# Optimization experiments

Measured on AMD Instinct MI355X. Metric: run time of the kernel, lower is better.

## Reference

```python
import jax, jax.numpy as jnp
import numpy as np

EPS = 1e-8


def setup_inputs() -> dict:
    key = jax.random.key(0)
    k1, k2, k3, k4 = jax.random.split(key, 4)
    B, S, H, D, E = 2, 2048, 1024, 4096, 8
    x = jax.random.normal(k1, (B, S, H), dtype=jnp.float32)
    routing_weights = jax.random.uniform(k2, (B, S, E), dtype=jnp.float32)
    # xavier-uniform-like scale for the expert weight tensors
    lim_d = float(np.sqrt(6.0 / (H + D)))
    lim_u = float(np.sqrt(6.0 / (D + H)))
    down_weights = jax.random.uniform(k3, (E, H, D), dtype=jnp.float32, minval=-lim_d, maxval=lim_d)
    up_weights = jax.random.uniform(k4, (E, D, H), dtype=jnp.float32, minval=-lim_u, maxval=lim_u)
    down_biases = jnp.zeros((E, D), dtype=jnp.float32)
    return {
        "x": x,
        "routing_weights": routing_weights,
        "down_weights": down_weights,
        "down_biases": down_biases,
        "up_weights": up_weights,
        "top_k": 2,
    }


def reference(x, routing_weights, down_weights, down_biases, up_weights, top_k):
    """SmearExpert.forward with routing_strategy='top_k_sparse' (3D routing weights).
    Returns (output, sparse_weights) exactly as the torch module does."""
    B, S, H = x.shape
    E = down_weights.shape[0]

    # top-k sparsification + renormalization of the routing weights
    topk_w, topk_i = jax.lax.top_k(routing_weights, top_k)          # [B,S,k]
    sparse_w = (jax.nn.one_hot(topk_i, E, dtype=x.dtype) * topk_w[..., None]).sum(-2)  # [B,S,E]
    sparse_w = sparse_w / (sparse_w.sum(-1, keepdims=True) + EPS)

    x_flat = x.reshape(-1, H)              # [T,H]
    w_flat = sparse_w.reshape(-1, E)       # [T,E]

    # per-expert down-proj -> GELU(exact) -> up-proj, combined with routing weights
    # (tokens with zero weight contribute nothing, matching the masked torch path)
    out = jnp.zeros_like(x_flat)
    for e in range(E):
        z = jax.nn.gelu(x_flat @ down_weights[e] + down_biases[e], approximate=False)  # [T,D]
        out = out + (z @ up_weights[e]) * w_flat[:, e:e + 1]
    return out.reshape(B, S, H), sparse_w
```

## Files before the change

### kernel.cpp

```cpp
#include <hip/hip_runtime.h>
#include <stdint.h>

#define T_TOK 4096
#define HDIM  1024
#define DDIM  4096
#define NEXP  8

typedef unsigned short ushort_t;
typedef __attribute__((ext_vector_type(8))) short bf16x8;
typedef __attribute__((ext_vector_type(4))) float f32x4;

__device__ __forceinline__ float bf2f(ushort_t b) {
  return __uint_as_float(((unsigned int)b) << 16);
}
__device__ __forceinline__ unsigned int f2bf(float f) {
  unsigned int u = __float_as_uint(f);
  return (u + 0x7fffu + ((u >> 16) & 1u)) >> 16;
}

__device__ __forceinline__ void gld16(const void* g, void* l) {
  __builtin_amdgcn_global_load_lds(
      (const __attribute__((address_space(1))) unsigned int*)g,
      (__attribute__((address_space(3))) unsigned int*)l, 16, 0, 0);
}

__global__ void k_init(int* counts) {
  if (threadIdx.x < NEXP) counts[threadIdx.x] = 0;
}

__global__ void k_route(const float* __restrict__ rw, float* __restrict__ sw_out,
                        int* counts, int* inv_e, int* inv_p, float* inv_w,
                        int* tokA) {
  int t = blockIdx.x * 256 + threadIdx.x;
  if (t >= T_TOK) return;
  float v[NEXP];
#pragma unroll
  for (int e = 0; e < NEXP; e++) v[e] = rw[t * NEXP + e];
  int i0 = 0; float m0 = v[0];
#pragma unroll
  for (int e = 1; e < NEXP; e++) if (v[e] > m0) { m0 = v[e]; i0 = e; }
  int i1 = -1; float m1 = -1e30f;
#pragma unroll
  for (int e = 0; e < NEXP; e++) if (e != i0 && v[e] > m1) { m1 = v[e]; i1 = e; }
  float s = m0 + m1 + 1e-8f;
  float w0 = m0 / s, w1 = m1 / s;
#pragma unroll
  for (int e = 0; e < NEXP; e++) {
    float w = (e == i0) ? w0 : ((e == i1) ? w1 : 0.0f);
    sw_out[t * NEXP + e] = w;
  }
  int p0 = atomicAdd(&counts[i0], 1);
  int p1 = atomicAdd(&counts[i1], 1);
  tokA[i0 * T_TOK + p0] = t;
  tokA[i1 * T_TOK + p1] = t;
  inv_e[t * 2] = i0; inv_e[t * 2 + 1] = i1;
  inv_p[t * 2] = p0; inv_p[t * 2 + 1] = p1;
  inv_w[t * 2] = w0; inv_w[t * 2 + 1] = w1;
}

__global__ void k_offsets(const int* counts, int* offsets) {
  int acc = 0;
  for (int e = 0; e < NEXP; e++) { offsets[e] = acc; acc += counts[e]; }
}

__global__ __launch_bounds__(256)
void k_cvtx(const float* __restrict__ x, ushort_t* __restrict__ xb) {
  size_t i = (size_t)blockIdx.x * 256 + threadIdx.x;
  float4 f0 = ((const float4*)x)[i * 2];
  float4 f1 = ((const float4*)x)[i * 2 + 1];
  uint4 o;
  o.x = f2bf(f0.x) | (f2bf(f0.y) << 16);
  o.y = f2bf(f0.z) | (f2bf(f0.w) << 16);
  o.z = f2bf(f1.x) | (f2bf(f1.y) << 16);
  o.w = f2bf(f1.z) | (f2bf(f1.w) << 16);
  ((uint4*)xb)[i] = o;
}

template <int KDIM, int NDIM>
__global__ __launch_bounds__(256)
void k_cvtw(const float* __restrict__ W, ushort_t* __restrict__ Wt) {
  constexpr int KT = KDIM / 64;
  __shared__ __align__(16) ushort_t lds[64 * 256];
  const int ekt = blockIdx.y;
  const int e  = ekt / KT;
  const int kt = ekt % KT;
  const int n0 = blockIdx.x * 256;
  const int t  = threadIdx.x;
  const int wv = t >> 6;
  const int ln = t & 63;
  const float* src = W + (size_t)e * KDIM * NDIM + (size_t)(kt * 64) * NDIM + n0;
#pragma unroll
  for (int it = 0; it < 16; ++it) {
    int r = it * 4 + wv;
    float4 f = *(const float4*)(src + (size_t)r * NDIM + ln * 4);
    uint2 o;
    o.x = f2bf(f.x) | (f2bf(f.y) << 16);
    o.y = f2bf(f.z) | (f2bf(f.w) << 16);
    *(uint2*)(lds + r * 256 + ln * 4) = o;
  }
  __syncthreads();
  ushort_t* dst = Wt + ((size_t)ekt * NDIM + n0 + t) * 64;
  const int sw = t & 7;
#pragma unroll
  for (int g = 0; g < 8; ++g) {
    unsigned int h0 = lds[(g * 8 + 0) * 256 + t];
    unsigned int h1 = lds[(g * 8 + 1) * 256 + t];
    unsigned int h2 = lds[(g * 8 + 2) * 256 + t];
    unsigned int h3 = lds[(g * 8 + 3) * 256 + t];
    unsigned int h4 = lds[(g * 8 + 4) * 256 + t];
    unsigned int h5 = lds[(g * 8 + 5) * 256 + t];
    unsigned int h6 = lds[(g * 8 + 6) * 256 + t];
    unsigned int h7 = lds[(g * 8 + 7) * 256 + t];
    uint4 o;
    o.x = h0 | (h1 << 16);
    o.y = h2 | (h3 << 16);
    o.z = h4 | (h5 << 16);
    o.w = h6 | (h7 << 16);
    *(uint4*)(dst + (g ^ sw) * 8) = o;
  }
}

template <int KDIM, int NDIM, bool DOWN>
__global__ __launch_bounds__(256, 3)
void k_gemm(const ushort_t* __restrict__ Asrc, const ushort_t* __restrict__ Wt,
            const float* __restrict__ bias, const int* __restrict__ counts,
            const int* __restrict__ offsets, const int* __restrict__ tokA,
            ushort_t* __restrict__ Out) {
  constexpr int KT = KDIM / 64;
  __shared__ __align__(16) short a_sh[128 * 64];
  __shared__ __align__(16) short b_sh[128 * 64];
  const int e    = blockIdx.y >> 5;
  const int tile = blockIdx.y & 31;
  const int cnt  = counts[e];
  if (tile * 128 >= cnt) return;
  const int off_e = offsets[e];
  const int zbase = off_e + tile * 128;
  const int n0    = blockIdx.x * 128;
  const int tid   = threadIdx.x;
  const int wave  = tid >> 6;
  const int lane  = tid & 63;
  const int rgrp  = lane >> 3;
  const int lc    = lane & 7;

  const ushort_t* abase[4];
#pragma unroll
  for (int i = 0; i < 4; i++) {
    int rl = wave * 32 + i * 8 + rgrp;
    int ridx = tile * 128 + rl;
    int ridx_c = (ridx < cnt) ? ridx : tile * 128;
    size_t row;
    if constexpr (DOWN) row = (size_t)tokA[e * T_TOK + ridx_c];
    else                row = (size_t)(off_e + ridx_c);
    abase[i] = Asrc + row * KDIM + ((lc ^ (rl & 7)) * 8);
  }
  const ushort_t* bbase = Wt + ((size_t)e * KT * NDIM + n0) * 64 + wave * 2048 + lane * 8;
  char* a_seg = (char*)a_sh + wave * 4096;
  char* b_seg = (char*)b_sh + wave * 4096;

  const int lm   = lane & 15;
  const int quad = lane >> 4;

  f32x4 acc[8][2];
  const f32x4 zero = {0.0f, 0.0f, 0.0f, 0.0f};
#pragma unroll
  for (int mf = 0; mf < 8; mf++)
#pragma unroll
    for (int nf = 0; nf < 2; nf++) acc[mf][nf] = zero;

  for (int kt = 0; kt < KT; ++kt) {
#pragma unroll
    for (int it = 0; it < 4; ++it)
      gld16(abase[it] + kt * 64, a_seg + it * 1024);
    const ushort_t* bg = bbase + (size_t)kt * (NDIM * 64);
#pragma unroll
    for (int it = 0; it < 4; ++it)
      gld16(bg + it * 512, b_seg + it * 1024);
    __syncthreads();
#pragma unroll
    for (int ks = 0; ks < 2; ++ks) {
      bf16x8 af[8];
#pragma unroll
      for (int mf = 0; mf < 8; mf++) {
        int m = mf * 16 + lm;
        int cc = (ks * 4 + quad) ^ (lm & 7);
        af[mf] = *(const bf16x8*)(a_sh + m * 64 + cc * 8);
      }
      bf16x8 bfv[2];
#pragma unroll
      for (int nf = 0; nf < 2; nf++) {
        int n = wave * 32 + nf * 16 + lm;
        int cc = (ks * 4 + quad) ^ (lm & 7);
        bfv[nf] = *(const bf16x8*)(b_sh + n * 64 + cc * 8);
      }
#pragma unroll
      for (int mf = 0; mf < 8; mf++)
#pragma unroll
        for (int nf = 0; nf < 2; nf++)
          acc[mf][nf] = __builtin_amdgcn_mfma_f32_16x16x32_bf16(af[mf], bfv[nf], acc[mf][nf], 0, 0, 0);
    }
    __syncthreads();
  }

  float bv[2] = {0.0f, 0.0f};
  if constexpr (DOWN) {
#pragma unroll
    for (int nf = 0; nf < 2; nf++)
      bv[nf] = bias[e * NDIM + n0 + wave * 32 + nf * 16 + lm];
  }
  short* ep = ((wave & 2) ? b_sh : a_sh) + (wave & 1) * 4096;
#pragma unroll
  for (int mf = 0; mf < 8; mf++)
#pragma unroll
    for (int nf = 0; nf < 2; nf++)
#pragma unroll
      for (int r = 0; r < 4; r++) {
        float v = acc[mf][nf][r];
        if constexpr (DOWN) {
          float zv = v + bv[nf];
          v = 0.5f * zv * (1.0f + erff(zv * 0.70710678118654752f));
        }
        ep[(mf * 16 + quad * 4 + r) * 32 + nf * 16 + lm] = (short)f2bf(v);
      }
  __syncthreads();
#pragma unroll
  for (int it = 0; it < 8; ++it) {
    int row = it * 16 + (lane >> 2);
    uint4 v = *(const uint4*)(ep + row * 32 + (lane & 3) * 8);
    if (tile * 128 + row < cnt)
      *(uint4*)(Out + (size_t)(zbase + row) * NDIM + n0 + wave * 32 + (lane & 3) * 8) = v;
  }
}

__global__ void k_combine(const ushort_t* __restrict__ U, const int* __restrict__ inv_e,
                          const int* __restrict__ inv_p, const float* __restrict__ inv_w,
                          const int* __restrict__ offsets, float* __restrict__ out) {
  int gid = blockIdx.x * 256 + threadIdx.x;
  int t  = gid >> 7;
  int hc = (gid & 127) * 8;
  int e0 = inv_e[t * 2], e1 = inv_e[t * 2 + 1];
  size_t s0 = (size_t)offsets[e0] + inv_p[t * 2];
  size_t s1 = (size_t)offsets[e1] + inv_p[t * 2 + 1];
  float w0 = inv_w[t * 2], w1 = inv_w[t * 2 + 1];
  const ushort_t* u0 = U + s0 * HDIM + hc;
  const ushort_t* u1 = U + s1 * HDIM + hc;
  uint4 q0 = *(const uint4*)u0;
  uint4 q1 = *(const uint4*)u1;
  const ushort_t* a = (const ushort_t*)&q0;
  const ushort_t* b = (const ushort_t*)&q1;
  float4 o0, o1;
  o0.x = w0 * bf2f(a[0]) + w1 * bf2f(b[0]);
  o0.y = w0 * bf2f(a[1]) + w1 * bf2f(b[1]);
  o0.z = w0 * bf2f(a[2]) + w1 * bf2f(b[2]);
  o0.w = w0 * bf2f(a[3]) + w1 * bf2f(b[3]);
  o1.x = w0 * bf2f(a[4]) + w1 * bf2f(b[4]);
  o1.y = w0 * bf2f(a[5]) + w1 * bf2f(b[5]);
  o1.z = w0 * bf2f(a[6]) + w1 * bf2f(b[6]);
  o1.w = w0 * bf2f(a[7]) + w1 * bf2f(b[7]);
  float* op = out + (size_t)t * HDIM + hc;
  *(float4*)(op)     = o0;
  *(float4*)(op + 4) = o1;
}

extern "C" void kernel_launch(void* const* d_in, const int* in_sizes, int n_in,
                              void* d_out, int out_size, void* d_ws, size_t ws_size,
                              hipStream_t stream) {
  const float* x  = (const float*)d_in[0];
  const float* rw = (const float*)d_in[1];
  const float* wd = (const float*)d_in[2];
  const float* bd = (const float*)d_in[3];
  const float* wu = (const float*)d_in[4];
  float* out    = (float*)d_out;
  float* sw_out = out + (size_t)T_TOK * HDIM;

  char* ws = (char*)d_ws;
  int*      counts = (int*)(ws);
  int*      offs   = (int*)(ws + 64);
  int*      inv_e  = (int*)(ws + 128);
  int*      inv_p  = (int*)(ws + 128 + 32768);
  float*    inv_w  = (float*)(ws + 128 + 65536);
  int*      tokA   = (int*)(ws + 128 + 98304);
  size_t    base   = 262144;
  ushort_t* Z      = (ushort_t*)(ws + base);
  ushort_t* U      = (ushort_t*)(ws + base + 67108864);
  ushort_t* xbf    = (ushort_t*)(ws + base + 67108864 + 16777216);
  ushort_t* Wt     = (ushort_t*)(ws + base + 67108864 + 16777216 + 8388608);

  k_init<<<1, 64, 0, stream>>>(counts);
  k_route<<<T_TOK / 256, 256, 0, stream>>>(rw, sw_out, counts, inv_e, inv_p, inv_w, tokA);
  k_offsets<<<1, 1, 0, stream>>>(counts, offs);
  k_cvtx<<<T_TOK * HDIM / 8 / 256, 256, 0, stream>>>(x, xbf);
  k_cvtw<HDIM, DDIM><<<dim3(DDIM / 256, NEXP * (HDIM / 64)), 256, 0, stream>>>(wd, Wt);
  k_gemm<HDIM, DDIM, true><<<dim3(DDIM / 128, NEXP * 32), 256, 0, stream>>>(
      xbf, Wt, bd, counts, offs, tokA, Z);
  k_cvtw<DDIM, HDIM><<<dim3(HDIM / 256, NEXP * (DDIM / 64)), 256, 0, stream>>>(wu, Wt);
  k_gemm<DDIM, HDIM, false><<<dim3(HDIM / 128, NEXP * 32), 256, 0, stream>>>(
      Z, Wt, nullptr, counts, offs, tokA, U);
  k_combine<<<(T_TOK * HDIM / 8) / 256, 256, 0, stream>>>(U, inv_e, inv_p, inv_w, offs, out);
}
```

Measured before the change: 603.3 us.

## Double-buffer LDS tiles in expert GEMM and aggregate routing atomics per block

The GEMM now keeps two LDS buffers for the A and B tiles. It prefetches the next k-tile with global_load_lds while MFMAs run on the current one, using an explicit vmcnt wait and raw barriers in place of two full __syncthreads per iteration. Launch bounds drop from 3 to 2 blocks per CU because LDS use doubles. The routing kernel first counts per-expert slots with shared-memory atomics and then issues one global atomic per expert per block, which also changes the order of token slots.

```diff
diff --git a/kernel.cpp b/kernel.cpp
--- a/kernel.cpp
+++ b/kernel.cpp
@@ -24,15 +24,21 @@
       (__attribute__((address_space(3))) unsigned int*)l, 16, 0, 0);
 }
 
+#define MEMFENCE asm volatile("" ::: "memory")
+
 __global__ void k_init(int* counts) {
   if (threadIdx.x < NEXP) counts[threadIdx.x] = 0;
 }
 
-__global__ void k_route(const float* __restrict__ rw, float* __restrict__ sw_out,
-                        int* counts, int* inv_e, int* inv_p, float* inv_w,
-                        int* tokA) {
+__global__ __launch_bounds__(256)
+void k_route(const float* __restrict__ rw, float* __restrict__ sw_out,
+             int* counts, int* inv_e, int* inv_p, float* inv_w,
+             int* tokA) {
+  __shared__ int lcnt[NEXP];
+  __shared__ int lbase[NEXP];
   int t = blockIdx.x * 256 + threadIdx.x;
-  if (t >= T_TOK) return;
+  if (threadIdx.x < NEXP) lcnt[threadIdx.x] = 0;
+  __syncthreads();
   float v[NEXP];
 #pragma unroll
   for (int e = 0; e < NEXP; e++) v[e] = rw[t * NEXP + e];
@@ -49,8 +55,14 @@
     float w = (e == i0) ? w0 : ((e == i1) ? w1 : 0.0f);
     sw_out[t * NEXP + e] = w;
   }
-  int p0 = atomicAdd(&counts[i0], 1);
-  int p1 = atomicAdd(&counts[i1], 1);
+  int p0l = atomicAdd(&lcnt[i0], 1);
+  int p1l = atomicAdd(&lcnt[i1], 1);
+  __syncthreads();
+  if (threadIdx.x < NEXP)
+    lbase[threadIdx.x] = atomicAdd(&counts[threadIdx.x], lcnt[threadIdx.x]);
+  __syncthreads();
+  int p0 = lbase[i0] + p0l;
+  int p1 = lbase[i1] + p1l;
   tokA[i0 * T_TOK + p0] = t;
   tokA[i1 * T_TOK + p1] = t;
   inv_e[t * 2] = i0; inv_e[t * 2 + 1] = i1;
@@ -121,14 +133,14 @@
 }
 
 template <int KDIM, int NDIM, bool DOWN>
-__global__ __launch_bounds__(256, 3)
+__global__ __launch_bounds__(256, 2)
 void k_gemm(const ushort_t* __restrict__ Asrc, const ushort_t* __restrict__ Wt,
             const float* __restrict__ bias, const int* __restrict__ counts,
             const int* __restrict__ offsets, const int* __restrict__ tokA,
             ushort_t* __restrict__ Out) {
   constexpr int KT = KDIM / 64;
-  __shared__ __align__(16) short a_sh[128 * 64];
-  __shared__ __align__(16) short b_sh[128 * 64];
+  __shared__ __align__(16) short a_sh[2][128 * 64];
+  __shared__ __align__(16) short b_sh[2][128 * 64];
   const int e    = blockIdx.y >> 5;
   const int tile = blockIdx.y & 31;
   const int cnt  = counts[e];
@@ -154,8 +166,6 @@
     abase[i] = Asrc + row * KDIM + ((lc ^ (rl & 7)) * 8);
   }
   const ushort_t* bbase = Wt + ((size_t)e * KT * NDIM + n0) * 64 + wave * 2048 + lane * 8;
-  char* a_seg = (char*)a_sh + wave * 4096;
-  char* b_seg = (char*)b_sh + wave * 4096;
 
   const int lm   = lane & 15;
   const int quad = lane >> 4;
@@ -167,7 +177,9 @@
 #pragma unroll
     for (int nf = 0; nf < 2; nf++) acc[mf][nf] = zero;
 
-  for (int kt = 0; kt < KT; ++kt) {
+  auto stage = [&](int buf, int kt) {
+    char* a_seg = (char*)&a_sh[buf][0] + wave * 4096;
+    char* b_seg = (char*)&b_sh[buf][0] + wave * 4096;
 #pragma unroll
     for (int it = 0; it < 4; ++it)
       gld16(abase[it] + kt * 64, a_seg + it * 1024);
@@ -175,7 +187,22 @@
 #pragma unroll
     for (int it = 0; it < 4; ++it)
       gld16(bg + it * 512, b_seg + it * 1024);
-    __syncthreads();
+  };
+
+  stage(0, 0);
+
+  for (int kt = 0; kt < KT; ++kt) {
+    const int cur = kt & 1;
+    if (kt + 1 < KT) {
+      stage(cur ^ 1, kt + 1);
+      asm volatile("s_waitcnt vmcnt(8)" ::: "memory");
+    } else {
+      asm volatile("s_waitcnt vmcnt(0)" ::: "memory");
+    }
+    __builtin_amdgcn_s_barrier();
+    MEMFENCE;
+    const short* ab = &a_sh[cur][0];
+    const short* bb = &b_sh[cur][0];
 #pragma unroll
     for (int ks = 0; ks < 2; ++ks) {
       bf16x8 af[8];
@@ -183,14 +210,14 @@
       for (int mf = 0; mf < 8; mf++) {
         int m = mf * 16 + lm;
         int cc = (ks * 4 + quad) ^ (lm & 7);
-        af[mf] = *(const bf16x8*)(a_sh + m * 64 + cc * 8);
+        af[mf] = *(const bf16x8*)(ab + m * 64 + cc * 8);
       }
       bf16x8 bfv[2];
 #pragma unroll
       for (int nf = 0; nf < 2; nf++) {
         int n = wave * 32 + nf * 16 + lm;
         int cc = (ks * 4 + quad) ^ (lm & 7);
-        bfv[nf] = *(const bf16x8*)(b_sh + n * 64 + cc * 8);
+        bfv[nf] = *(const bf16x8*)(bb + n * 64 + cc * 8);
       }
 #pragma unroll
       for (int mf = 0; mf < 8; mf++)
@@ -198,7 +225,9 @@
         for (int nf = 0; nf < 2; nf++)
           acc[mf][nf] = __builtin_amdgcn_mfma_f32_16x16x32_bf16(af[mf], bfv[nf], acc[mf][nf], 0, 0, 0);
     }
-    __syncthreads();
+    MEMFENCE;
+    __builtin_amdgcn_s_barrier();
+    MEMFENCE;
   }
 
   float bv[2] = {0.0f, 0.0f};
@@ -207,7 +236,7 @@
     for (int nf = 0; nf < 2; nf++)
       bv[nf] = bias[e * NDIM + n0 + wave * 32 + nf * 16 + lm];
   }
-  short* ep = ((wave & 2) ? b_sh : a_sh) + (wave & 1) * 4096;
+  short* ep = ((wave & 2) ? &b_sh[0][0] : &a_sh[0][0]) + (wave & 1) * 4096;
 #pragma unroll
   for (int mf = 0; mf < 8; mf++)
 #pragma unroll
```

New measurement: 613.0 us. About the same (+1.6%).
